# Performance work log

Measured on AMD Instinct MI355X. Metric: run time of the kernel, lower is better.

The kernel has to match this reference:

```python
import jax, jax.numpy as jnp
import numpy as np

SEQ_LEN, IN_CH, OUT_CH, H, BATCH = 2048, 16, 1, 80, 512


def _lstm(x, W_ih, W_hh, b_ih, b_hh):
    """Single-layer batch-first LSTM (PyTorch gate order i,f,g,o).
    x: [B, T, D]. Returns (outputs [B, T, H], last hidden [B, H])."""
    B = x.shape[0]
    h0 = jnp.zeros((B, H), x.dtype)
    c0 = jnp.zeros((B, H), x.dtype)
    # Precompute input projections for all timesteps in one GEMM: [T, B, 4H]
    xproj = jnp.einsum('btd,gd->tbg', x, W_ih) + (b_ih + b_hh)

    def step(carry, xp_t):
        h, c = carry
        gates = xp_t + h @ W_hh.T  # [B, 4H]
        i, f, g, o = jnp.split(gates, 4, axis=-1)
        i = jax.nn.sigmoid(i)
        f = jax.nn.sigmoid(f)
        g = jnp.tanh(g)
        o = jax.nn.sigmoid(o)
        c = f * c + i * g
        h = o * jnp.tanh(c)
        return (h, c), h

    (h_last, _), hs = jax.lax.scan(step, (h0, c0), xproj)
    return jnp.swapaxes(hs, 0, 1), h_last


def setup_inputs() -> dict:
    key = jax.random.key(0)
    ks = jax.random.split(key, 12)
    s1 = 1.0 / np.sqrt(H)
    d = {
        'x': jax.random.normal(ks[0], (BATCH, SEQ_LEN, IN_CH), jnp.float32),
        'W_ih1': jax.random.uniform(ks[1], (4 * H, IN_CH), jnp.float32, -s1, s1),
        'W_hh1': jax.random.uniform(ks[2], (4 * H, H), jnp.float32, -s1, s1),
        'b_ih1': jax.random.uniform(ks[3], (4 * H,), jnp.float32, -s1, s1),
        'b_hh1': jax.random.uniform(ks[4], (4 * H,), jnp.float32, -s1, s1),
        'W_ih2': jax.random.uniform(ks[5], (4 * H, H), jnp.float32, -s1, s1),
        'W_hh2': jax.random.uniform(ks[6], (4 * H, H), jnp.float32, -s1, s1),
        'b_ih2': jax.random.uniform(ks[7], (4 * H,), jnp.float32, -s1, s1),
        'b_hh2': jax.random.uniform(ks[8], (4 * H,), jnp.float32, -s1, s1),
        'W_d': jax.random.uniform(ks[9], (OUT_CH, H), jnp.float32, -s1, s1),
        'b_d': jax.random.uniform(ks[10], (OUT_CH,), jnp.float32, -s1, s1),
    }
    return d


def reference(x, W_ih1, W_hh1, b_ih1, b_hh1, W_ih2, W_hh2, b_ih2, b_hh2, W_d, b_d):
    B = x.shape[0]
    x = x.reshape((B, SEQ_LEN, IN_CH))
    y1, _ = _lstm(x, W_ih1, W_hh1, b_ih1, b_hh1)          # [B, T, H]
    _, h_last = _lstm(y1, W_ih2, W_hh2, b_ih2, b_hh2)     # [B, H]
    return h_last @ W_d.T + b_d                           # [B, OUT_CH]
```

## Files before the change

kernel.cpp:

```cpp
#include <hip/hip_runtime.h>

#define T_SEQ 2048
#define DIN   16
#define HH    80
#define NTHR  512
#define NBLK  256
#define BT    2
#define ROWE  192

#define L2E   1.44269504088896340736f

typedef _Float16 f16x8 __attribute__((ext_vector_type(8)));
typedef float    f32x4 __attribute__((ext_vector_type(4)));

__device__ __forceinline__ float rcp_fast(float x){ return __builtin_amdgcn_rcpf(x); }
__device__ __forceinline__ float ex2(float x){
#if __has_builtin(__builtin_amdgcn_exp2f)
    return __builtin_amdgcn_exp2f(x);
#else
    return exp2f(x);
#endif
}

#define MFMA16(ac, av, bv) ac = __builtin_amdgcn_mfma_f32_16x16x32_f16(av, bv, ac, 0, 0, 0)

__global__
__attribute__((amdgpu_flat_work_group_size(NTHR, NTHR)))
__attribute__((amdgpu_waves_per_eu(2, 2)))
void lstm2_mfma(
    const float* __restrict__ x,
    const float* __restrict__ W_ih1, const float* __restrict__ W_hh1,
    const float* __restrict__ b_ih1, const float* __restrict__ b_hh1,
    const float* __restrict__ W_ih2, const float* __restrict__ W_hh2,
    const float* __restrict__ b_ih2, const float* __restrict__ b_hh2,
    const float* __restrict__ W_d,   const float* __restrict__ b_d,
    float* __restrict__ out)
{
    __shared__ __align__(16) _Float16 HB[2][BT][ROWE];

    const int t    = threadIdx.x;
    const int lane = t & 63;
    const int wv   = t >> 6;
    const bool isL1w = (wv < 4);
    const int m16  = lane & 15;
    const int kgrp = lane >> 4;
    const int b0   = blockIdx.x * BT;

    const int uloc = isL1w ? 20*wv : 20*(wv-4);

    f16x8 A[5][5];
    {
        const int g  = m16 & 3;
        const int ut = m16 >> 2;
        const float sc = (g == 2) ? (2.f*L2E) : L2E;
        #pragma unroll
        for (int tl = 0; tl < 5; ++tl) {
            const int grow = g*HH + (uloc + 4*tl + ut);
            if (isL1w) {
                #pragma unroll
                for (int c = 0; c < 3; ++c) {
                    f16x8 a;
                    #pragma unroll
                    for (int j = 0; j < 8; ++j) {
                        const int k = 32*c + 8*kgrp + j;
                        const float v = (k < DIN) ? W_ih1[grow*DIN + k]
                                                  : W_hh1[grow*HH + (k - DIN)];
                        a[j] = (_Float16)(v * sc);
                    }
                    A[tl][c] = a;
                }
            } else {
                #pragma unroll
                for (int c = 0; c < 5; ++c) {
                    f16x8 a;
                    #pragma unroll
                    for (int j = 0; j < 8; ++j) {
                        const int k = 32*c + 8*kgrp + j;
                        const float v = (k < HH) ? W_ih2[grow*HH + k]
                                                 : W_hh2[grow*HH + (k - HH)];
                        a[j] = (_Float16)(v * sc);
                    }
                    A[tl][c] = a;
                }
            }
        }
    }

    const int  tl_ep    = m16 >> 1;
    const bool act_ep   = (m16 < 10);
    const int  unit_ep  = uloc + 4*(act_ep ? tl_ep : 0) + kgrp;
    const int  batch_ep = lane & 1;
    const int  seg      = isL1w ? DIN : (DIN + HH);
    const float* bI  = isL1w ? b_ih1 : b_ih2;
    const float* bHh = isL1w ? b_hh1 : b_hh2;
    const float bi = (bI[      unit_ep] + bHh[      unit_ep]) * L2E;
    const float bf = (bI[ 80 + unit_ep] + bHh[ 80 + unit_ep]) * L2E;
    const float bg = (bI[160 + unit_ep] + bHh[160 + unit_ep]) * (2.f*L2E);
    const float bo = (bI[240 + unit_ep] + bHh[240 + unit_ep]) * L2E;

    for (int i = t; i < 2*BT*ROWE; i += NTHR) ((_Float16*)HB)[i] = (_Float16)0.f;
    __syncthreads();

    const int xbn = (lane >> 4) & 1;
    const int xch = lane & 15;
    const float* xptr = x + ((size_t)(b0 + xbn) * T_SEQ) * DIN + xch;
    float xa = 0.f, xbv = 0.f, xcv = 0.f;
    if (wv == 0 && lane < 32) {
        HB[0][xbn][xch] = (_Float16)xptr[0];
        xa  = xptr[1*DIN];
        xbv = xptr[2*DIN];
        xcv = xptr[3*DIN];
    }
    __syncthreads();

    float cst = 0.f;

    #pragma unroll 1
    for (int k = 0; k <= T_SEQ; ++k) {
        const int pb = k & 1, nb = pb ^ 1;

        if (wv == 0 && lane < 32) {
            HB[nb][xbn][xch] = (_Float16)xa;
            xa = xbv; xbv = xcv;
            const int tn = (k + 4 < T_SEQ) ? (k + 4) : (T_SEQ - 1);
            xcv = xptr[(size_t)tn * DIN];
        }

        const bool act = isL1w ? (k < T_SEQ) : (k >= 1);
        if (act) {
            const _Float16* rb = &HB[pb][lane & 1][0];
            f32x4 acc0 = {0.f,0.f,0.f,0.f}, acc1 = {0.f,0.f,0.f,0.f},
                  acc2 = {0.f,0.f,0.f,0.f}, acc3 = {0.f,0.f,0.f,0.f},
                  acc4 = {0.f,0.f,0.f,0.f};

            if (isL1w) {
                const f16x8 B0 = *(const f16x8*)(rb +       8*kgrp);
                const f16x8 B1 = *(const f16x8*)(rb +  32 + 8*kgrp);
                const f16x8 B2 = *(const f16x8*)(rb +  64 + 8*kgrp);
                MFMA16(acc0, A[0][0], B0); MFMA16(acc0, A[0][1], B1); MFMA16(acc0, A[0][2], B2);
                MFMA16(acc1, A[1][0], B0); MFMA16(acc1, A[1][1], B1); MFMA16(acc1, A[1][2], B2);
                MFMA16(acc2, A[2][0], B0); MFMA16(acc2, A[2][1], B1); MFMA16(acc2, A[2][2], B2);
                MFMA16(acc3, A[3][0], B0); MFMA16(acc3, A[3][1], B1); MFMA16(acc3, A[3][2], B2);
                MFMA16(acc4, A[4][0], B0); MFMA16(acc4, A[4][1], B1); MFMA16(acc4, A[4][2], B2);
            } else {
                const f16x8 B0 = *(const f16x8*)(rb +  16 + 8*kgrp);
                const f16x8 B1 = *(const f16x8*)(rb +  48 + 8*kgrp);
                const f16x8 B2 = *(const f16x8*)(rb +  80 + 8*kgrp);
                const f16x8 B3 = *(const f16x8*)(rb + 112 + 8*kgrp);
                const f16x8 B4 = *(const f16x8*)(rb + 144 + 8*kgrp);
                MFMA16(acc0, A[0][0], B0); MFMA16(acc0, A[0][1], B1); MFMA16(acc0, A[0][2], B2);
                MFMA16(acc0, A[0][3], B3); MFMA16(acc0, A[0][4], B4);
                MFMA16(acc1, A[1][0], B0); MFMA16(acc1, A[1][1], B1); MFMA16(acc1, A[1][2], B2);
                MFMA16(acc1, A[1][3], B3); MFMA16(acc1, A[1][4], B4);
                MFMA16(acc2, A[2][0], B0); MFMA16(acc2, A[2][1], B1); MFMA16(acc2, A[2][2], B2);
                MFMA16(acc2, A[2][3], B3); MFMA16(acc2, A[2][4], B4);
                MFMA16(acc3, A[3][0], B0); MFMA16(acc3, A[3][1], B1); MFMA16(acc3, A[3][2], B2);
                MFMA16(acc3, A[3][3], B3); MFMA16(acc3, A[3][4], B4);
                MFMA16(acc4, A[4][0], B0); MFMA16(acc4, A[4][1], B1); MFMA16(acc4, A[4][2], B2);
                MFMA16(acc4, A[4][3], B3); MFMA16(acc4, A[4][4], B4);
            }

            float M0 = acc0[0], M1 = acc0[1], M2 = acc0[2], M3 = acc0[3];
            if (tl_ep == 1) { M0 = acc1[0]; M1 = acc1[1]; M2 = acc1[2]; M3 = acc1[3]; }
            if (tl_ep == 2) { M0 = acc2[0]; M1 = acc2[1]; M2 = acc2[2]; M3 = acc2[3]; }
            if (tl_ep == 3) { M0 = acc3[0]; M1 = acc3[1]; M2 = acc3[2]; M3 = acc3[3]; }
            if (tl_ep == 4) { M0 = acc4[0]; M1 = acc4[1]; M2 = acc4[2]; M3 = acc4[3]; }

            const float gi = M0 + bi, gf = M1 + bf, gg = M2 + bg, go = M3 + bo;
            const float iv = rcp_fast(1.f + ex2(-gi));
            const float fv = rcp_fast(1.f + ex2(-gf));
            const float ov = rcp_fast(1.f + ex2(-go));
            const float gv = 1.f - 2.f*rcp_fast(1.f + ex2(gg));
            cst = fv*cst + iv*gv;
            const float tc = 1.f - 2.f*rcp_fast(1.f + ex2(cst * (2.f*L2E)));
            if (act_ep) HB[nb][batch_ep][seg + unit_ep] = (_Float16)(ov * tc);
        }
        __syncthreads();
    }

    if (wv == 0) {
        float a0 = 0.f, a1 = 0.f;
        for (int u = lane; u < HH; u += 64) {
            const float wd = W_d[u];
            a0 += wd * (float)HB[1][0][DIN + HH + u];
            a1 += wd * (float)HB[1][1][DIN + HH + u];
        }
        #pragma unroll
        for (int off = 32; off > 0; off >>= 1) {
            a0 += __shfl_down(a0, off);
            a1 += __shfl_down(a1, off);
        }
        if (lane == 0) { out[b0] = a0 + b_d[0]; out[b0 + 1] = a1 + b_d[0]; }
    }
}

extern "C" void kernel_launch(void* const* d_in, const int* in_sizes, int n_in,
                              void* d_out, int out_size, void* d_ws, size_t ws_size,
                              hipStream_t stream) {
    const float* x     = (const float*)d_in[0];
    const float* W_ih1 = (const float*)d_in[1];
    const float* W_hh1 = (const float*)d_in[2];
    const float* b_ih1 = (const float*)d_in[3];
    const float* b_hh1 = (const float*)d_in[4];
    const float* W_ih2 = (const float*)d_in[5];
    const float* W_hh2 = (const float*)d_in[6];
    const float* b_ih2 = (const float*)d_in[7];
    const float* b_hh2 = (const float*)d_in[8];
    const float* W_d   = (const float*)d_in[9];
    const float* b_d   = (const float*)d_in[10];

    lstm2_mfma<<<NBLK, NTHR, 0, stream>>>(x, W_ih1, W_hh1, b_ih1, b_hh1,
                                          W_ih2, W_hh2, b_ih2, b_hh2,
                                          W_d, b_d, (float*)d_out);
}
```

Before: 1.330 ms.

## Software-pipeline the two LSTM layers across a split-phase barrier per step

Each timestep is split into two phases separated by an extra barrier. Layer-2 waves start their MFMA on the x/h1 slice early and defer their epilogue by one step, and layer-1 runs its epilogue after the mid barrier. The aim is to overlap layer-2's long dot products with layer-1's gate math and shorten the serial critical path per timestep. MFMA sections also get raised wave priority. The cost is an extra barrier per step and a longer pipeline that runs one more iteration.

```diff
diff --git a/kernel.cpp b/kernel.cpp
--- a/kernel.cpp
+++ b/kernel.cpp
@@ -22,7 +22,8 @@
 #endif
 }
 
-#define MFMA16(ac, av, bv) ac = __builtin_amdgcn_mfma_f32_16x16x32_f16(av, bv, ac, 0, 0, 0)
+#define MFMA_ACC(ac, av, bv) ac = __builtin_amdgcn_mfma_f32_16x16x32_f16(av, bv, ac, 0, 0, 0)
+#define MFMA_NEW(av, bv)     __builtin_amdgcn_mfma_f32_16x16x32_f16(av, bv, zf4, 0, 0, 0)
 
 __global__
 __attribute__((amdgpu_flat_work_group_size(NTHR, NTHR)))
@@ -114,9 +115,27 @@
     __syncthreads();
 
     float cst = 0.f;
+    const f32x4 zf4 = {0.f,0.f,0.f,0.f};
+    f32x4 acc0 = zf4, acc1 = zf4, acc2 = zf4, acc3 = zf4, acc4 = zf4;
+
+    auto epilogue = [&](int par) {
+        float M0 = acc0[0], M1 = acc0[1], M2 = acc0[2], M3 = acc0[3];
+        if (tl_ep == 1) { M0 = acc1[0]; M1 = acc1[1]; M2 = acc1[2]; M3 = acc1[3]; }
+        if (tl_ep == 2) { M0 = acc2[0]; M1 = acc2[1]; M2 = acc2[2]; M3 = acc2[3]; }
+        if (tl_ep == 3) { M0 = acc3[0]; M1 = acc3[1]; M2 = acc3[2]; M3 = acc3[3]; }
+        if (tl_ep == 4) { M0 = acc4[0]; M1 = acc4[1]; M2 = acc4[2]; M3 = acc4[3]; }
+        const float gi = M0 + bi, gf = M1 + bf, gg = M2 + bg, go = M3 + bo;
+        const float iv = rcp_fast(1.f + ex2(-gi));
+        const float fv = rcp_fast(1.f + ex2(-gf));
+        const float ov = rcp_fast(1.f + ex2(-go));
+        const float gv = 1.f - 2.f*rcp_fast(1.f + ex2(gg));
+        cst = fv*cst + iv*gv;
+        const float tc = 1.f - 2.f*rcp_fast(1.f + ex2(cst * (2.f*L2E)));
+        if (act_ep) HB[par][batch_ep][seg + unit_ep] = (_Float16)(ov * tc);
+    };
 
     #pragma unroll 1
-    for (int k = 0; k <= T_SEQ; ++k) {
+    for (int k = 0; k <= T_SEQ + 1; ++k) {
         const int pb = k & 1, nb = pb ^ 1;
 
         if (wv == 0 && lane < 32) {
@@ -126,54 +145,61 @@
             xcv = xptr[(size_t)tn * DIN];
         }
 
-        const bool act = isL1w ? (k < T_SEQ) : (k >= 1);
-        if (act) {
-            const _Float16* rb = &HB[pb][lane & 1][0];
-            f32x4 acc0 = {0.f,0.f,0.f,0.f}, acc1 = {0.f,0.f,0.f,0.f},
-                  acc2 = {0.f,0.f,0.f,0.f}, acc3 = {0.f,0.f,0.f,0.f},
-                  acc4 = {0.f,0.f,0.f,0.f};
-
-            if (isL1w) {
+        if (isL1w) {
+            if (k < T_SEQ) {
+                const _Float16* rb = &HB[pb][lane & 1][0];
                 const f16x8 B0 = *(const f16x8*)(rb +       8*kgrp);
                 const f16x8 B1 = *(const f16x8*)(rb +  32 + 8*kgrp);
                 const f16x8 B2 = *(const f16x8*)(rb +  64 + 8*kgrp);
-                MFMA16(acc0, A[0][0], B0); MFMA16(acc0, A[0][1], B1); MFMA16(acc0, A[0][2], B2);
-                MFMA16(acc1, A[1][0], B0); MFMA16(acc1, A[1][1], B1); MFMA16(acc1, A[1][2], B2);
-                MFMA16(acc2, A[2][0], B0); MFMA16(acc2, A[2][1], B1); MFMA16(acc2, A[2][2], B2);
-                MFMA16(acc3, A[3][0], B0); MFMA16(acc3, A[3][1], B1); MFMA16(acc3, A[3][2], B2);
-                MFMA16(acc4, A[4][0], B0); MFMA16(acc4, A[4][1], B1); MFMA16(acc4, A[4][2], B2);
-            } else {
-                const f16x8 B0 = *(const f16x8*)(rb +  16 + 8*kgrp);
+                __builtin_amdgcn_s_setprio(1);
+                acc0 = MFMA_NEW(A[0][0], B0); MFMA_ACC(acc0, A[0][1], B1); MFMA_ACC(acc0, A[0][2], B2);
+                acc1 = MFMA_NEW(A[1][0], B0); MFMA_ACC(acc1, A[1][1], B1); MFMA_ACC(acc1, A[1][2], B2);
+                acc2 = MFMA_NEW(A[2][0], B0); MFMA_ACC(acc2, A[2][1], B1); MFMA_ACC(acc2, A[2][2], B2);
+                acc3 = MFMA_NEW(A[3][0], B0); MFMA_ACC(acc3, A[3][1], B1); MFMA_ACC(acc3, A[3][2], B2);
+                acc4 = MFMA_NEW(A[4][0], B0); MFMA_ACC(acc4, A[4][1], B1); MFMA_ACC(acc4, A[4][2], B2);
+                __builtin_amdgcn_s_setprio(0);
+            }
+        } else {
+            if (k >= 2) epilogue(pb);
+            if (k >= 1 && k <= T_SEQ) {
+                const _Float16* rb = &HB[pb][lane & 1][0];
+                const f16x8 B0 = *(const f16x8*)(rb + 16 + 8*kgrp);
+                __builtin_amdgcn_s_setprio(1);
+                acc0 = MFMA_NEW(A[0][0], B0);
+                acc1 = MFMA_NEW(A[1][0], B0);
+                acc2 = MFMA_NEW(A[2][0], B0);
+                acc3 = MFMA_NEW(A[3][0], B0);
+                acc4 = MFMA_NEW(A[4][0], B0);
+                __builtin_amdgcn_s_setprio(0);
+            }
+        }
+
+        asm volatile("s_waitcnt lgkmcnt(0)" ::: "memory");
+        __builtin_amdgcn_s_barrier();
+        __builtin_amdgcn_sched_barrier(0);
+
+        if (isL1w) {
+            if (k < T_SEQ) epilogue(nb);
+        } else {
+            if (k >= 1 && k <= T_SEQ) {
+                const _Float16* rb = &HB[pb][lane & 1][0];
                 const f16x8 B1 = *(const f16x8*)(rb +  48 + 8*kgrp);
                 const f16x8 B2 = *(const f16x8*)(rb +  80 + 8*kgrp);
                 const f16x8 B3 = *(const f16x8*)(rb + 112 + 8*kgrp);
                 const f16x8 B4 = *(const f16x8*)(rb + 144 + 8*kgrp);
-                MFMA16(acc0, A[0][0], B0); MFMA16(acc0, A[0][1], B1); MFMA16(acc0, A[0][2], B2);
-                MFMA16(acc0, A[0][3], B3); MFMA16(acc0, A[0][4], B4);
-                MFMA16(acc1, A[1][0], B0); MFMA16(acc1, A[1][1], B1); MFMA16(acc1, A[1][2], B2);
-                MFMA16(acc1, A[1][3], B3); MFMA16(acc1, A[1][4], B4);
-                MFMA16(acc2, A[2][0], B0); MFMA16(acc2, A[2][1], B1); MFMA16(acc2, A[2][2], B2);
-                MFMA16(acc2, A[2][3], B3); MFMA16(acc2, A[2][4], B4);
-                MFMA16(acc3, A[3][0], B0); MFMA16(acc3, A[3][1], B1); MFMA16(acc3, A[3][2], B2);
-                MFMA16(acc3, A[3][3], B3); MFMA16(acc3, A[3][4], B4);
-                MFMA16(acc4, A[4][0], B0); MFMA16(acc4, A[4][1], B1); MFMA16(acc4, A[4][2], B2);
-                MFMA16(acc4, A[4][3], B3); MFMA16(acc4, A[4][4], B4);
-            }
-
-            float M0 = acc0[0], M1 = acc0[1], M2 = acc0[2], M3 = acc0[3];
-            if (tl_ep == 1) { M0 = acc1[0]; M1 = acc1[1]; M2 = acc1[2]; M3 = acc1[3]; }
-            if (tl_ep == 2) { M0 = acc2[0]; M1 = acc2[1]; M2 = acc2[2]; M3 = acc2[3]; }
-            if (tl_ep == 3) { M0 = acc3[0]; M1 = acc3[1]; M2 = acc3[2]; M3 = acc3[3]; }
-            if (tl_ep == 4) { M0 = acc4[0]; M1 = acc4[1]; M2 = acc4[2]; M3 = acc4[3]; }
-
-            const float gi = M0 + bi, gf = M1 + bf, gg = M2 + bg, go = M3 + bo;
-            const float iv = rcp_fast(1.f + ex2(-gi));
-            const float fv = rcp_fast(1.f + ex2(-gf));
-            const float ov = rcp_fast(1.f + ex2(-go));
-            const float gv = 1.f - 2.f*rcp_fast(1.f + ex2(gg));
-            cst = fv*cst + iv*gv;
-            const float tc = 1.f - 2.f*rcp_fast(1.f + ex2(cst * (2.f*L2E)));
-            if (act_ep) HB[nb][batch_ep][seg + unit_ep] = (_Float16)(ov * tc);
+                __builtin_amdgcn_s_setprio(1);
+                MFMA_ACC(acc0, A[0][1], B1); MFMA_ACC(acc0, A[0][2], B2);
+                MFMA_ACC(acc0, A[0][3], B3); MFMA_ACC(acc0, A[0][4], B4);
+                MFMA_ACC(acc1, A[1][1], B1); MFMA_ACC(acc1, A[1][2], B2);
+                MFMA_ACC(acc1, A[1][3], B3); MFMA_ACC(acc1, A[1][4], B4);
+                MFMA_ACC(acc2, A[2][1], B1); MFMA_ACC(acc2, A[2][2], B2);
+                MFMA_ACC(acc2, A[2][3], B3); MFMA_ACC(acc2, A[2][4], B4);
+                MFMA_ACC(acc3, A[3][1], B1); MFMA_ACC(acc3, A[3][2], B2);
+                MFMA_ACC(acc3, A[3][3], B3); MFMA_ACC(acc3, A[3][4], B4);
+                MFMA_ACC(acc4, A[4][1], B1); MFMA_ACC(acc4, A[4][2], B2);
+                MFMA_ACC(acc4, A[4][3], B3); MFMA_ACC(acc4, A[4][4], B4);
+                __builtin_amdgcn_s_setprio(0);
+            }
         }
         __syncthreads();
     }
```

Measured after the change: 1.549 ms. 1.16x slower.

## Balance MFMA work across waves by mixing layer-1 and layer-2 tiles per wave

Applied to the files above, without the earlier changes.

Before, waves 0-3 handled only layer 1 (3 MFMAs per tile) and waves 4-7 only layer 2 (5 MFMAs per tile), so the per-step barrier waited on the heavier layer-2 waves. Now each wave owns a mix of layer-1 and layer-2 gate tiles so MFMA counts per wave are nearly equal. The bias is also folded into the accumulator init, which removes the separate adds. The cost is that every wave now reads both sets of B operands from shared memory and the indexing is more complex. The k==0 and k==T_SEQ edge cases are handled with a cup predicate, and the layer-1 tail step now writes an extra value.

```diff
diff --git a/kernel.cpp b/kernel.cpp
--- a/kernel.cpp
+++ b/kernel.cpp
@@ -22,7 +22,13 @@
 #endif
 }
 
-#define MFMA16(ac, av, bv) ac = __builtin_amdgcn_mfma_f32_16x16x32_f16(av, bv, ac, 0, 0, 0)
+#define MF(av, bv, cv) __builtin_amdgcn_mfma_f32_16x16x32_f16(av, bv, cv, 0, 0, 0)
+
+#define L1SLOT(acc, s) { acc = MF(A[s][0], BL0, BIAS[s]); acc = MF(A[s][1], BL1, acc); \
+                         acc = MF(A[s][2], BL2, acc); }
+#define L2SLOT(acc, s) { acc = MF(A[s][0], BM0, BIAS[s]); acc = MF(A[s][1], BM1, acc); \
+                         acc = MF(A[s][2], BM2, acc); acc = MF(A[s][3], BM3, acc); \
+                         acc = MF(A[s][4], BM4, acc); }
 
 __global__
 __attribute__((amdgpu_flat_work_group_size(NTHR, NTHR)))
@@ -41,62 +47,59 @@
     const int t    = threadIdx.x;
     const int lane = t & 63;
     const int wv   = t >> 6;
-    const bool isL1w = (wv < 4);
     const int m16  = lane & 15;
     const int kgrp = lane >> 4;
     const int b0   = blockIdx.x * BT;
 
-    const int uloc = isL1w ? 20*wv : 20*(wv-4);
+    const int nL1 = (wv < 4) ? 3 : 2;
+    const int l1b = (wv < 4) ? 3*wv : 12 + 2*(wv-4);
+    const int l2b = (wv < 4) ? 2*wv :  8 + 3*(wv-4);
 
     f16x8 A[5][5];
+    f32x4 BIAS[5];
     {
         const int g  = m16 & 3;
         const int ut = m16 >> 2;
         const float sc = (g == 2) ? (2.f*L2E) : L2E;
         #pragma unroll
-        for (int tl = 0; tl < 5; ++tl) {
-            const int grow = g*HH + (uloc + 4*tl + ut);
-            if (isL1w) {
+        for (int s = 0; s < 5; ++s) {
+            const bool sl1 = (s < nL1);
+            const int  gt  = sl1 ? (l1b + s) : (l2b + (s - nL1));
+            const int  grow = g*HH + 4*gt + ut;
+            #pragma unroll
+            for (int c = 0; c < 5; ++c) {
+                if (sl1 && c >= 3) continue;
+                f16x8 a;
                 #pragma unroll
-                for (int c = 0; c < 3; ++c) {
-                    f16x8 a;
-                    #pragma unroll
-                    for (int j = 0; j < 8; ++j) {
-                        const int k = 32*c + 8*kgrp + j;
-                        const float v = (k < DIN) ? W_ih1[grow*DIN + k]
-                                                  : W_hh1[grow*HH + (k - DIN)];
-                        a[j] = (_Float16)(v * sc);
-                    }
-                    A[tl][c] = a;
+                for (int j = 0; j < 8; ++j) {
+                    const int k = 32*c + 8*kgrp + j;
+                    const float v = sl1
+                        ? ((k < DIN) ? W_ih1[grow*DIN + k] : W_hh1[grow*HH + (k - DIN)])
+                        : ((k < HH)  ? W_ih2[grow*HH  + k] : W_hh2[grow*HH + (k - HH)]);
+                    a[j] = (_Float16)(v * sc);
                 }
-            } else {
-                #pragma unroll
-                for (int c = 0; c < 5; ++c) {
-                    f16x8 a;
-                    #pragma unroll
-                    for (int j = 0; j < 8; ++j) {
-                        const int k = 32*c + 8*kgrp + j;
-                        const float v = (k < HH) ? W_ih2[grow*HH + k]
-                                                 : W_hh2[grow*HH + (k - HH)];
-                        a[j] = (_Float16)(v * sc);
-                    }
-                    A[tl][c] = a;
-                }
+                A[s][c] = a;
             }
-        }
-    }
-
-    const int  tl_ep    = m16 >> 1;
-    const bool act_ep   = (m16 < 10);
-    const int  unit_ep  = uloc + 4*(act_ep ? tl_ep : 0) + kgrp;
+            const int u = 4*gt + kgrp;
+            const float* bI = sl1 ? b_ih1 : b_ih2;
+            const float* bH = sl1 ? b_hh1 : b_hh2;
+            f32x4 bb;
+            bb[0] = (bI[       u] + bH[       u]) * L2E;
+            bb[1] = (bI[ 80  + u] + bH[ 80  + u]) * L2E;
+            bb[2] = (bI[160  + u] + bH[160  + u]) * (2.f*L2E);
+            bb[3] = (bI[240  + u] + bH[240  + u]) * L2E;
+            BIAS[s] = bb;
+        }
+    }
+
+    const int  te      = m16 >> 1;
+    const bool act_ep  = (m16 < 10);
+    const int  sE      = act_ep ? te : 0;
+    const bool eL1     = (sE < nL1);
+    const int  gtE     = eL1 ? (l1b + sE) : (l2b + (sE - nL1));
+    const int  unit_ep = 4*gtE + kgrp;
+    const int  seg     = eL1 ? DIN : (DIN + HH);
     const int  batch_ep = lane & 1;
-    const int  seg      = isL1w ? DIN : (DIN + HH);
-    const float* bI  = isL1w ? b_ih1 : b_ih2;
-    const float* bHh = isL1w ? b_hh1 : b_hh2;
-    const float bi = (bI[      unit_ep] + bHh[      unit_ep]) * L2E;
-    const float bf = (bI[ 80 + unit_ep] + bHh[ 80 + unit_ep]) * L2E;
-    const float bg = (bI[160 + unit_ep] + bHh[160 + unit_ep]) * (2.f*L2E);
-    const float bo = (bI[240 + unit_ep] + bHh[240 + unit_ep]) * L2E;
 
     for (int i = t; i < 2*BT*ROWE; i += NTHR) ((_Float16*)HB)[i] = (_Float16)0.f;
     __syncthreads();
@@ -126,55 +129,41 @@
             xcv = xptr[(size_t)tn * DIN];
         }
 
-        const bool act = isL1w ? (k < T_SEQ) : (k >= 1);
-        if (act) {
-            const _Float16* rb = &HB[pb][lane & 1][0];
-            f32x4 acc0 = {0.f,0.f,0.f,0.f}, acc1 = {0.f,0.f,0.f,0.f},
-                  acc2 = {0.f,0.f,0.f,0.f}, acc3 = {0.f,0.f,0.f,0.f},
-                  acc4 = {0.f,0.f,0.f,0.f};
-
-            if (isL1w) {
-                const f16x8 B0 = *(const f16x8*)(rb +       8*kgrp);
-                const f16x8 B1 = *(const f16x8*)(rb +  32 + 8*kgrp);
-                const f16x8 B2 = *(const f16x8*)(rb +  64 + 8*kgrp);
-                MFMA16(acc0, A[0][0], B0); MFMA16(acc0, A[0][1], B1); MFMA16(acc0, A[0][2], B2);
-                MFMA16(acc1, A[1][0], B0); MFMA16(acc1, A[1][1], B1); MFMA16(acc1, A[1][2], B2);
-                MFMA16(acc2, A[2][0], B0); MFMA16(acc2, A[2][1], B1); MFMA16(acc2, A[2][2], B2);
-                MFMA16(acc3, A[3][0], B0); MFMA16(acc3, A[3][1], B1); MFMA16(acc3, A[3][2], B2);
-                MFMA16(acc4, A[4][0], B0); MFMA16(acc4, A[4][1], B1); MFMA16(acc4, A[4][2], B2);
-            } else {
-                const f16x8 B0 = *(const f16x8*)(rb +  16 + 8*kgrp);
-                const f16x8 B1 = *(const f16x8*)(rb +  48 + 8*kgrp);
-                const f16x8 B2 = *(const f16x8*)(rb +  80 + 8*kgrp);
-                const f16x8 B3 = *(const f16x8*)(rb + 112 + 8*kgrp);
-                const f16x8 B4 = *(const f16x8*)(rb + 144 + 8*kgrp);
-                MFMA16(acc0, A[0][0], B0); MFMA16(acc0, A[0][1], B1); MFMA16(acc0, A[0][2], B2);
-                MFMA16(acc0, A[0][3], B3); MFMA16(acc0, A[0][4], B4);
-                MFMA16(acc1, A[1][0], B0); MFMA16(acc1, A[1][1], B1); MFMA16(acc1, A[1][2], B2);
-                MFMA16(acc1, A[1][3], B3); MFMA16(acc1, A[1][4], B4);
-                MFMA16(acc2, A[2][0], B0); MFMA16(acc2, A[2][1], B1); MFMA16(acc2, A[2][2], B2);
-                MFMA16(acc2, A[2][3], B3); MFMA16(acc2, A[2][4], B4);
-                MFMA16(acc3, A[3][0], B0); MFMA16(acc3, A[3][1], B1); MFMA16(acc3, A[3][2], B2);
-                MFMA16(acc3, A[3][3], B3); MFMA16(acc3, A[3][4], B4);
-                MFMA16(acc4, A[4][0], B0); MFMA16(acc4, A[4][1], B1); MFMA16(acc4, A[4][2], B2);
-                MFMA16(acc4, A[4][3], B3); MFMA16(acc4, A[4][4], B4);
-            }
-
-            float M0 = acc0[0], M1 = acc0[1], M2 = acc0[2], M3 = acc0[3];
-            if (tl_ep == 1) { M0 = acc1[0]; M1 = acc1[1]; M2 = acc1[2]; M3 = acc1[3]; }
-            if (tl_ep == 2) { M0 = acc2[0]; M1 = acc2[1]; M2 = acc2[2]; M3 = acc2[3]; }
-            if (tl_ep == 3) { M0 = acc3[0]; M1 = acc3[1]; M2 = acc3[2]; M3 = acc3[3]; }
-            if (tl_ep == 4) { M0 = acc4[0]; M1 = acc4[1]; M2 = acc4[2]; M3 = acc4[3]; }
-
-            const float gi = M0 + bi, gf = M1 + bf, gg = M2 + bg, go = M3 + bo;
-            const float iv = rcp_fast(1.f + ex2(-gi));
-            const float fv = rcp_fast(1.f + ex2(-gf));
-            const float ov = rcp_fast(1.f + ex2(-go));
-            const float gv = 1.f - 2.f*rcp_fast(1.f + ex2(gg));
-            cst = fv*cst + iv*gv;
-            const float tc = 1.f - 2.f*rcp_fast(1.f + ex2(cst * (2.f*L2E)));
-            if (act_ep) HB[nb][batch_ep][seg + unit_ep] = (_Float16)(ov * tc);
-        }
+        const _Float16* rb = &HB[pb][lane & 1][0];
+        const f16x8 BL0 = *(const f16x8*)(rb +       8*kgrp);
+        const f16x8 BL1 = *(const f16x8*)(rb +  32 + 8*kgrp);
+        const f16x8 BL2 = *(const f16x8*)(rb +  64 + 8*kgrp);
+        const f16x8 BM0 = *(const f16x8*)(rb +  16 + 8*kgrp);
+        const f16x8 BM1 = *(const f16x8*)(rb +  48 + 8*kgrp);
+        const f16x8 BM2 = *(const f16x8*)(rb +  80 + 8*kgrp);
+        const f16x8 BM3 = *(const f16x8*)(rb + 112 + 8*kgrp);
+        const f16x8 BM4 = *(const f16x8*)(rb + 144 + 8*kgrp);
+
+        f32x4 acc0, acc1, acc2, acc3, acc4;
+        if (wv < 4) {
+            L1SLOT(acc0, 0) L1SLOT(acc1, 1) L1SLOT(acc2, 2)
+            L2SLOT(acc3, 3) L2SLOT(acc4, 4)
+        } else {
+            L1SLOT(acc0, 0) L1SLOT(acc1, 1)
+            L2SLOT(acc2, 2) L2SLOT(acc3, 3) L2SLOT(acc4, 4)
+        }
+
+        float M0 = acc0[0], M1 = acc0[1], M2 = acc0[2], M3 = acc0[3];
+        if (te == 1) { M0 = acc1[0]; M1 = acc1[1]; M2 = acc1[2]; M3 = acc1[3]; }
+        if (te == 2) { M0 = acc2[0]; M1 = acc2[1]; M2 = acc2[2]; M3 = acc2[3]; }
+        if (te == 3) { M0 = acc3[0]; M1 = acc3[1]; M2 = acc3[2]; M3 = acc3[3]; }
+        if (te == 4) { M0 = acc4[0]; M1 = acc4[1]; M2 = acc4[2]; M3 = acc4[3]; }
+
+        const float iv = rcp_fast(1.f + ex2(-M0));
+        const float fv = rcp_fast(1.f + ex2(-M1));
+        const float gv = 1.f - 2.f*rcp_fast(1.f + ex2(M2));
+        const float ov = rcp_fast(1.f + ex2(-M3));
+        const bool  cup = eL1 || (k > 0);
+        if (cup) cst = fv*cst + iv*gv;
+        const float tc = 1.f - 2.f*rcp_fast(1.f + ex2(cst * (2.f*L2E)));
+        if (act_ep && cup)
+            HB[nb][batch_ep][seg + unit_ep] = (_Float16)(ov * tc);
+
         __syncthreads();
     }
 
```

Result: no change. 1.346 ms (+1.2%).
